# Performance work log

Measured on AMD Instinct MI355X. Metric: run time of the kernel, lower is better.

The kernel has to match this reference:

```python
import jax, jax.numpy as jnp
import numpy as np
from functools import partial

IM_H, IM_W = 1024, 1024
PRE_NMS = 1000
POST_NMS = 1000
FPN_POST_NMS = 1000
NMS_THRESH = 0.7
MIN_SIZE = 0.0
XFORM_CLIP = float(np.log(1000.0 / 16.0))  # BoxCoder bbox_xform_clip
K_MIN, K_MAX, K0, S0 = 2, 5, 4, 224.0      # ROI->FPN level mapper
NEG_INF = -1.0e30
N_IMG = 8


def _make_anchors(H, W, stride, n_img):
    """Grid anchors in H,W,A order (matches permute(0,2,3,1) flattening)."""
    ratios = np.array([0.5, 1.0, 2.0])
    size = stride * 8.0
    ws = size * np.sqrt(1.0 / ratios)
    hs = size * np.sqrt(ratios)
    sx = (np.arange(W) + 0.5) * stride
    sy = (np.arange(H) + 0.5) * stride
    cx, cy = np.meshgrid(sx, sy)  # [H,W]
    x1 = cx[..., None] - ws / 2.0
    y1 = cy[..., None] - hs / 2.0
    x2 = cx[..., None] + ws / 2.0
    y2 = cy[..., None] + hs / 2.0
    anc = np.stack([x1, y1, x2, y2], -1).reshape(-1, 4).astype(np.float32)
    return jnp.asarray(np.broadcast_to(anc, (n_img,) + anc.shape).copy())


def setup_inputs() -> dict:
    key = jax.random.key(0)
    ks = jax.random.split(key, 6)
    inp = {
        "obj_p2": jax.random.normal(ks[0], (N_IMG, 3, 256, 256), jnp.float32),
        "obj_p3": jax.random.normal(ks[1], (N_IMG, 3, 128, 128), jnp.float32),
        "obj_p4": jax.random.normal(ks[2], (N_IMG, 3, 64, 64), jnp.float32),
        "breg_p2": jax.random.normal(ks[3], (N_IMG, 12, 256, 256), jnp.float32) * 0.25,
        "breg_p3": jax.random.normal(ks[4], (N_IMG, 12, 128, 128), jnp.float32) * 0.25,
        "breg_p4": jax.random.normal(ks[5], (N_IMG, 12, 64, 64), jnp.float32) * 0.25,
        "anchors_p2": _make_anchors(256, 256, 4, N_IMG),
        "anchors_p3": _make_anchors(128, 128, 8, N_IMG),
        "anchors_p4": _make_anchors(64, 64, 16, N_IMG),
    }
    return inp


def _decode(deltas, anchors):
    # BoxCoder(weights=(1,1,1,1)) decode with the detectron +1 convention
    w = anchors[..., 2] - anchors[..., 0] + 1.0
    h = anchors[..., 3] - anchors[..., 1] + 1.0
    cx = anchors[..., 0] + 0.5 * w
    cy = anchors[..., 1] + 0.5 * h
    dx, dy = deltas[..., 0], deltas[..., 1]
    dw = jnp.minimum(deltas[..., 2], XFORM_CLIP)
    dh = jnp.minimum(deltas[..., 3], XFORM_CLIP)
    pcx = dx * w + cx
    pcy = dy * h + cy
    pw = jnp.exp(dw) * w
    ph = jnp.exp(dh) * h
    return jnp.stack(
        [pcx - 0.5 * pw, pcy - 0.5 * ph, pcx + 0.5 * pw - 1.0, pcy + 0.5 * ph - 1.0], -1
    )


def _nms_keep(boxes, valid, thresh):
    # boxes [K,4] already sorted by score desc; greedy hard NMS -> keep mask
    x1, y1, x2, y2 = boxes[:, 0], boxes[:, 1], boxes[:, 2], boxes[:, 3]
    areas = (x2 - x1 + 1.0) * (y2 - y1 + 1.0)
    xx1 = jnp.maximum(x1[:, None], x1[None, :])
    yy1 = jnp.maximum(y1[:, None], y1[None, :])
    xx2 = jnp.minimum(x2[:, None], x2[None, :])
    yy2 = jnp.minimum(y2[:, None], y2[None, :])
    inter = jnp.clip(xx2 - xx1 + 1.0, 0.0) * jnp.clip(yy2 - yy1 + 1.0, 0.0)
    iou = inter / (areas[:, None] + areas[None, :] - inter)
    K = boxes.shape[0]
    js = jnp.arange(K)

    def body(i, keep):
        sup = keep[i] & (iou[i] > thresh) & (js > i)
        return keep & ~sup

    return jax.lax.fori_loop(0, K, body, valid)


def _per_level(obj, breg, anchors):
    N, A, H, W = obj.shape
    scores = jax.nn.sigmoid(obj.transpose(0, 2, 3, 1).reshape(N, -1))  # [N, HWA]
    deltas = breg.reshape(N, A, 4, H, W).transpose(0, 3, 4, 1, 2).reshape(N, -1, 4)
    k = min(PRE_NMS, scores.shape[1])
    s, idx = jax.lax.top_k(scores, k)  # sorted desc
    d = jnp.take_along_axis(deltas, idx[..., None], axis=1)
    a = jnp.take_along_axis(anchors, idx[..., None], axis=1)
    p = _decode(d, a)
    # clip to image (width-1 / height-1)
    p = jnp.stack(
        [
            jnp.clip(p[..., 0], 0.0, IM_W - 1.0),
            jnp.clip(p[..., 1], 0.0, IM_H - 1.0),
            jnp.clip(p[..., 2], 0.0, IM_W - 1.0),
            jnp.clip(p[..., 3], 0.0, IM_H - 1.0),
        ],
        -1,
    )
    ws = p[..., 2] - p[..., 0] + 1.0
    hs = p[..., 3] - p[..., 1] + 1.0
    xc = p[..., 0] + ws / 2.0
    yc = p[..., 1] + hs / 2.0
    valid = (ws >= MIN_SIZE) & (hs >= MIN_SIZE) & (xc < IM_W) & (yc < IM_H)
    keep = jax.vmap(partial(_nms_keep, thresh=NMS_THRESH))(p, valid)
    ms = jnp.where(keep, s, NEG_INF)
    s2, i2 = jax.lax.top_k(ms, min(POST_NMS, k))
    b2 = jnp.take_along_axis(p, i2[..., None], axis=1)
    return b2, s2


def reference(obj_p2, obj_p3, obj_p4, breg_p2, breg_p3, breg_p4,
              anchors_p2, anchors_p3, anchors_p4):
    levels_in = [
        (obj_p2, breg_p2, anchors_p2),
        (obj_p3, breg_p3, anchors_p3),
        (obj_p4, breg_p4, anchors_p4),
    ]
    bs, ss = zip(*[_per_level(o, b, a) for o, b, a in levels_in])
    boxes = jnp.concatenate(bs, axis=1)   # [N, L*POST_NMS, 4]
    scores = jnp.concatenate(ss, axis=1)  # [N, L*POST_NMS]
    pk = min(FPN_POST_NMS, scores.shape[1])
    fs, fi = jax.lax.top_k(scores, pk)    # per-image inference-mode topk
    fb = jnp.take_along_axis(boxes, fi[..., None], axis=1)
    # ROI -> FPN level mapping
    area = (fb[..., 2] - fb[..., 0] + 1.0) * (fb[..., 3] - fb[..., 1] + 1.0)
    lvl = jnp.floor(K0 + jnp.log2(jnp.sqrt(area) / S0 + 1e-6))
    lvl = jnp.clip(lvl, K_MIN, K_MAX).astype(jnp.int32)
    return fb, fs, lvl
```

## Files before the change

kernel.cpp:

```cpp
#include <hip/hip_runtime.h>

#define NTASK 24
#define KSEL 1000
#define NIMG 8
#define NEG_INF_D (-1e30)
#define CAND_CAP 2048


static __device__ __forceinline__ unsigned fkey(float x) {
    unsigned u = __float_as_uint(x);
    return u ^ ((u >> 31) ? 0xFFFFFFFFu : 0x80000000u);
}

static __device__ __forceinline__ unsigned long long dkey(double d) {
    unsigned long long u = (unsigned long long)__double_as_longlong(d);
    if (u >> 63) u = ~u; else u |= 0x8000000000000000ull;
    return u;
}

static __device__ __forceinline__ int level_hw(int lvl) {
    return lvl == 0 ? 65536 : (lvl == 1 ? 16384 : 4096);
}


__global__ __launch_bounds__(256) void k_zero(uint4* __restrict__ p, int n16) {
    const int t = blockIdx.x * 256 + threadIdx.x;
    if (t < n16) p[t] = make_uint4(0u, 0u, 0u, 0u);
}


__global__ __launch_bounds__(256) void k_hist(const float* __restrict__ o2,
                                              const float* __restrict__ o3,
                                              const float* __restrict__ o4,
                                              unsigned* __restrict__ hist) {
    const int task = blockIdx.x, img = task / 3, lvl = task % 3;
    const float* obj = lvl == 0 ? o2 : (lvl == 1 ? o3 : o4);
    const int HW = level_hw(lvl);
    const int total = 3 * HW;
    const float* base = obj + (size_t)img * total;
    const int tid = threadIdx.x;

    __shared__ unsigned h[4096];
    for (int t = tid; t < 4096; t += 256) h[t] = 0u;
    __syncthreads();

    const int per = total / 32;
    const int beg = blockIdx.y * per;
    for (int t = beg + tid; t < beg + per; t += 256) {
        unsigned key = fkey(base[t]);
        atomicAdd(&h[key >> 20], 1u);
    }
    __syncthreads();

    unsigned* H = hist + task * 4096;
    for (int t = tid; t < 4096; t += 256)
        if (h[t]) atomicAdd(&H[t], h[t]);
}


__global__ __launch_bounds__(256) void k_thresh(const unsigned* __restrict__ hist,
                                                int* __restrict__ thrBin) {
    const int task = blockIdx.x, tid = threadIdx.x;
    __shared__ unsigned h[4096];
    __shared__ unsigned part[256];
    const unsigned* H = hist + task * 4096;
    for (int t = tid; t < 4096; t += 256) h[t] = H[t];
    __syncthreads();
    unsigned s = 0;
    for (int q = 0; q < 16; ++q) s += h[tid * 16 + q];
    part[tid] = s;
    __syncthreads();
    if (tid == 0) {
        unsigned cum = 0;
        int c = 255;
        for (; c >= 0; --c) {
            if (cum + part[c] >= (unsigned)KSEL) break;
            cum += part[c];
        }
        if (c < 0) c = 0;
        int bin = 0;
        for (int b = c * 16 + 15; b >= c * 16; --b) {
            if (cum + h[b] >= (unsigned)KSEL) { bin = b; break; }
            cum += h[b];
        }
        thrBin[task] = bin;
    }
}


__global__ __launch_bounds__(256) void k_compact(const float* __restrict__ o2,
                                                 const float* __restrict__ o3,
                                                 const float* __restrict__ o4,
                                                 const int* __restrict__ thrBin,
                                                 unsigned* __restrict__ cnt,
                                                 unsigned long long* __restrict__ cand) {
    const int task = blockIdx.x, img = task / 3, lvl = task % 3;
    const float* obj = lvl == 0 ? o2 : (lvl == 1 ? o3 : o4);
    const int HW = level_hw(lvl);
    const int total = 3 * HW;
    const float* base = obj + (size_t)img * total;
    const unsigned B = (unsigned)thrBin[task];

    __shared__ unsigned long long buf[CAND_CAP];
    __shared__ unsigned scnt, sbase;
    if (threadIdx.x == 0) scnt = 0u;
    __syncthreads();

    const int per = total / 32;
    const int per4 = per >> 2;
    const int beg4 = blockIdx.y * per4;
    const float4* base4 = (const float4*)base;
    for (int t = beg4 + threadIdx.x; t < beg4 + per4; t += 256) {
        float4 v = base4[t];
        const int e0 = t * 4;
#pragma unroll
        for (int q = 0; q < 4; ++q) {
            float x = q == 0 ? v.x : (q == 1 ? v.y : (q == 2 ? v.z : v.w));
            unsigned key = fkey(x);
            if ((key >> 20) >= B) {
                unsigned s = atomicAdd(&scnt, 1u);
                if (s < CAND_CAP) {
                    int el = e0 + q;
                    int a = el / HW, pos = el - a * HW;
                    int i = pos * 3 + a;
                    buf[s] = ((unsigned long long)key << 32) | (unsigned)(~(unsigned)i);
                }
            }
        }
    }
    __syncthreads();
    unsigned n = scnt; if (n > CAND_CAP) n = CAND_CAP;
    if (threadIdx.x == 0) sbase = atomicAdd(&cnt[task], n);
    __syncthreads();
    const unsigned b0 = sbase;
    for (unsigned t = threadIdx.x; t < n; t += 256) {
        unsigned slot = b0 + t;
        if (slot < CAND_CAP) cand[task * CAND_CAP + slot] = buf[t];
    }
}


__global__ __launch_bounds__(1024) void k_sel(const unsigned* __restrict__ cnt,
                                              const unsigned long long* __restrict__ cand,
                                              int* __restrict__ idx_out) {
    const int task = blockIdx.x, tid = threadIdx.x;
    __shared__ unsigned long long comp[CAND_CAP];
    int n = (int)cnt[task]; if (n > CAND_CAP) n = CAND_CAP;
    for (int t = tid; t < CAND_CAP; t += 1024)
        comp[t] = (t < n) ? cand[task * CAND_CAP + t] : 0ull;
    __syncthreads();

    for (unsigned k = 2; k <= CAND_CAP; k <<= 1) {
        for (unsigned j = k >> 1; j > 0; j >>= 1) {
            for (unsigned i = tid; i < CAND_CAP; i += 1024) {
                unsigned ixj = i ^ j;
                if (ixj > i) {
                    unsigned long long A = comp[i], Bv = comp[ixj];
                    bool desc = ((i & k) == 0);
                    if ((A < Bv) == desc) { comp[i] = Bv; comp[ixj] = A; }
                }
            }
            __syncthreads();
        }
    }

    for (int t = tid; t < KSEL; t += 1024)
        idx_out[task * KSEL + t] = (int)(~(unsigned)(comp[t] & 0xFFFFFFFFull));
}


__global__ __launch_bounds__(256) void k_decode(const float* __restrict__ o2, const float* __restrict__ o3, const float* __restrict__ o4,
                                                const float* __restrict__ g2, const float* __restrict__ g3, const float* __restrict__ g4,
                                                const float* __restrict__ a2, const float* __restrict__ a3, const float* __restrict__ a4,
                                                const int* __restrict__ idx,
                                                double* __restrict__ boxes, double* __restrict__ score, int* __restrict__ valid) {
    const int task = blockIdx.x, img = task / 3, lvl = task % 3;
    const float* obj = lvl == 0 ? o2 : (lvl == 1 ? o3 : o4);
    const float* brg = lvl == 0 ? g2 : (lvl == 1 ? g3 : g4);
    const float* anc = lvl == 0 ? a2 : (lvl == 1 ? a3 : a4);
    const int HW = level_hw(lvl);
    const int N = HW * 3;
    const double XC = 4.135166556742356;

    const int r = blockIdx.y * 250 + threadIdx.x;
    if (threadIdx.x < 250 && r < KSEL) {
        int i = idx[task * KSEL + r];
        int a = i % 3, pos = i / 3;
        double x = (double)obj[(size_t)img * 3 * HW + (size_t)a * HW + pos];
        double s = 1.0 / (1.0 + exp(-x));

        const float* bb = brg + (size_t)img * 12 * HW + (size_t)(a * 4) * HW + pos;
        double dx = (double)bb[0];
        double dy = (double)bb[(size_t)HW];
        double dw = (double)bb[(size_t)2 * HW];
        double dh = (double)bb[(size_t)3 * HW];

        const float* an = anc + ((size_t)img * N + (size_t)i) * 4;
        double ax1 = an[0], ay1 = an[1], ax2 = an[2], ay2 = an[3];

        double w = ax2 - ax1 + 1.0, h = ay2 - ay1 + 1.0;
        double cx = ax1 + 0.5 * w, cy = ay1 + 0.5 * h;
        if (dw > XC) dw = XC;
        if (dh > XC) dh = XC;
        double pcx = dx * w + cx, pcy = dy * h + cy;
        double pw = exp(dw) * w, ph = exp(dh) * h;
        double x1 = pcx - 0.5 * pw, y1 = pcy - 0.5 * ph;
        double x2 = pcx + 0.5 * pw - 1.0, y2 = pcy + 0.5 * ph - 1.0;
        x1 = fmin(fmax(x1, 0.0), 1023.0);
        y1 = fmin(fmax(y1, 0.0), 1023.0);
        x2 = fmin(fmax(x2, 0.0), 1023.0);
        y2 = fmin(fmax(y2, 0.0), 1023.0);
        double ws_ = x2 - x1 + 1.0, hs_ = y2 - y1 + 1.0;
        double xc = x1 + ws_ / 2.0, yc = y1 + hs_ / 2.0;
        int v = (ws_ >= 0.0) && (hs_ >= 0.0) && (xc < 1024.0) && (yc < 1024.0);

        double* bo = boxes + (size_t)(task * KSEL + r) * 4;
        bo[0] = x1; bo[1] = y1; bo[2] = x2; bo[3] = y2;
        score[task * KSEL + r] = s;
        valid[task * KSEL + r] = v;
    }
}


__global__ __launch_bounds__(512) void k_mask(const double* __restrict__ boxes,
                                              unsigned long long* __restrict__ maskT) {
    const int task = blockIdx.x;
    const int wid = threadIdx.x >> 6, lane = threadIdx.x & 63;
    const int t = blockIdx.y * 8 + wid;
    if (t >= 136) return;
    int I = 0, rem = t;
    while (rem >= 16 - I) { rem -= 16 - I; ++I; }
    const int J = I + rem;

    const double* B = boxes + (size_t)task * KSEL * 4;
    const int j = J * 64 + lane;
    const int jc = j < KSEL ? j : KSEL - 1;
    double jx1 = B[jc * 4 + 0], jy1 = B[jc * 4 + 1];
    double jx2 = B[jc * 4 + 2], jy2 = B[jc * 4 + 3];
    double aj = (jx2 - jx1 + 1.0) * (jy2 - jy1 + 1.0);

    unsigned long long* MT = maskT + (size_t)task * 16000 + (size_t)J * KSEL;
    int iend = I * 64 + 64; if (iend > KSEL) iend = KSEL;
    for (int i = I * 64; i < iend; ++i) {
        double ix1 = B[i * 4 + 0], iy1 = B[i * 4 + 1];
        double ix2 = B[i * 4 + 2], iy2 = B[i * 4 + 3];
        double ai = (ix2 - ix1 + 1.0) * (iy2 - iy1 + 1.0);
        double xx1 = fmax(ix1, jx1), yy1 = fmax(iy1, jy1);
        double xx2 = fmin(ix2, jx2), yy2 = fmin(iy2, jy2);
        double iw = xx2 - xx1 + 1.0; iw = iw > 0.0 ? iw : 0.0;
        double ih = yy2 - yy1 + 1.0; ih = ih > 0.0 ? ih : 0.0;
        double inter = iw * ih;
        double iou = inter / (ai + aj - inter);
        bool sup = (j > i) && (j < KSEL) && (iou > 0.7);
        unsigned long long m = __ballot(sup);
        if (lane == 0) MT[i] = m;
    }
}


__global__ __launch_bounds__(1024) void k_nms(const unsigned long long* __restrict__ maskT,
                                              const int* __restrict__ valid,
                                              const double* __restrict__ score,
                                              int* __restrict__ order, double* __restrict__ s2) {
    const int task = blockIdx.x;
    const int tid = threadIdx.x;
    const int wid = tid >> 6, lane = tid & 63;

    __shared__ unsigned long long Msh[16000];
    __shared__ unsigned long long kws[16];
    __shared__ int prefK[16], prefN[16], totKsh;

    {
        const ulonglong2* MG = (const ulonglong2*)(maskT + (size_t)task * 16000);
        ulonglong2* ML = (ulonglong2*)Msh;
        for (int t = tid; t < 8000; t += 1024) ML[t] = MG[t];
    }
    if (tid < 16) kws[tid] = 0ull;
    __syncthreads();
    if (tid < KSEL && valid[task * KSEL + tid])
        atomicOr(&kws[tid >> 6], 1ull << (tid & 63));
    __syncthreads();

    for (int p = 0; p < 16; ++p) {
        if (p > 0 && wid >= p) {
            unsigned long long kp = kws[p - 1];
            unsigned long long m = ((kp >> lane) & 1ull) ? Msh[wid * KSEL + (p - 1) * 64 + lane] : 0ull;
            if (m) atomicAnd(&kws[wid], ~m);
        }
        if (wid == p) {
            __threadfence_block();
            const int row = p * 64 + lane;
            unsigned long long m = (row < KSEL) ? Msh[p * KSEL + row] : 0ull;
            unsigned long long k = kws[p];
            unsigned long long processed = 0ull;
            while (true) {
                unsigned long long sup = __ballot((m & k) != 0ull);
                unsigned long long rem = k & sup & ~processed;
                if (!rem) break;
                int b = __ffsll((long long)rem) - 1;
                unsigned lo = (unsigned)__builtin_amdgcn_readlane((int)(unsigned)(m & 0xFFFFFFFFull), b);
                unsigned hi = (unsigned)__builtin_amdgcn_readlane((int)(unsigned)(m >> 32), b);
                unsigned long long vict = ((unsigned long long)hi << 32) | lo;
                k &= ~vict;
                processed = (1ull << b) | ((1ull << b) - 1ull);
            }
            if (lane == 0) kws[p] = k;
        }
        __syncthreads();
    }

    if (tid == 0) {
        int pk = 0, pn = 0;
        for (int l = 0; l < 16; ++l) {
            prefK[l] = pk; prefN[l] = pn;
            int limit = KSEL - 64 * l; if (limit > 64) limit = 64;
            int kb = (int)__popcll(kws[l]);
            pk += kb; pn += limit - kb;
        }
        totKsh = pk;
    }
    __syncthreads();

    if (tid < 16) {
        unsigned long long kw = kws[tid];
        int limit = KSEL - 64 * tid; if (limit > 64) limit = 64;
        int ck = prefK[tid], cn = totKsh + prefN[tid];
        for (int b = 0; b < limit; ++b) {
            int j = tid * 64 + b;
            if ((kw >> b) & 1ull) {
                order[task * KSEL + ck] = j;
                s2[task * KSEL + ck] = score[task * KSEL + j];
                ++ck;
            } else {
                order[task * KSEL + cn] = j;
                s2[task * KSEL + cn] = NEG_INF_D;
                ++cn;
            }
        }
    }
}


__global__ __launch_bounds__(1024) void k_final(const double* __restrict__ boxes,
                                                const double* __restrict__ s2,
                                                const int* __restrict__ order,
                                                float* __restrict__ out) {
    const int img = blockIdx.x;
    const int tid = threadIdx.x;
    __shared__ unsigned long long Mkey[KSEL];
    __shared__ int Mid[KSEL];

    const double* L0 = s2 + (size_t)(img * 3 + 0) * KSEL;
    const double* L1 = s2 + (size_t)(img * 3 + 1) * KSEL;
    const double* L2 = s2 + (size_t)(img * 3 + 2) * KSEL;

    if (tid < KSEL) {
        const int r = tid;
        int lo = 0, hi = r;
        while (lo < hi) {
            int a = (lo + hi) >> 1;
            if (dkey(L0[a]) >= dkey(L1[r - 1 - a])) lo = a + 1; else hi = a;
        }
        int a = lo, b = r - a;
        unsigned long long ka = dkey(L0[a]), kb = dkey(L1[b]);
        if (ka >= kb) { Mkey[r] = ka; Mid[r] = a; }
        else          { Mkey[r] = kb; Mid[r] = 1000 + b; }
    }
    __syncthreads();

    if (tid < KSEL) {
        const int r = tid;
        int lo = 0, hi = r;
        while (lo < hi) {
            int a = (lo + hi) >> 1;
            if (Mkey[a] >= dkey(L2[r - 1 - a])) lo = a + 1; else hi = a;
        }
        int a = lo, b = r - a;
        int e;
        if (a < KSEL && Mkey[a] >= dkey(L2[b])) e = Mid[a];
        else e = 2000 + b;

        int l = e / 1000, rr = e - l * 1000;
        int task = img * 3 + l;
        int pos = order[task * KSEL + rr];
        const double* bo = boxes + (size_t)(task * KSEL + pos) * 4;
        double b0 = bo[0], b1 = bo[1], b2 = bo[2], b3 = bo[3];
        double s = s2[task * KSEL + rr];

        float* fb = out + ((size_t)img * KSEL + r) * 4;
        fb[0] = (float)b0; fb[1] = (float)b1; fb[2] = (float)b2; fb[3] = (float)b3;
        out[8 * KSEL * 4 + img * KSEL + r] = (float)s;

        double area = (b2 - b0 + 1.0) * (b3 - b1 + 1.0);
        double lv = floor(4.0 + log2(sqrt(area) / 224.0 + 1e-6));
        if (!(lv >= 2.0)) lv = 2.0;
        if (lv > 5.0) lv = 5.0;
        out[8 * KSEL * 5 + img * KSEL + r] = (float)lv;
    }
}


extern "C" void kernel_launch(void* const* d_in, const int* in_sizes, int n_in,
                              void* d_out, int out_size, void* d_ws, size_t ws_size,
                              hipStream_t stream) {
    const float* o2 = (const float*)d_in[0];
    const float* o3 = (const float*)d_in[1];
    const float* o4 = (const float*)d_in[2];
    const float* g2 = (const float*)d_in[3];
    const float* g3 = (const float*)d_in[4];
    const float* g4 = (const float*)d_in[5];
    const float* a2 = (const float*)d_in[6];
    const float* a3 = (const float*)d_in[7];
    const float* a4 = (const float*)d_in[8];

    char* ws = (char*)d_ws;
    int*                idx   = (int*)(ws + 0);
    int*                valid = (int*)(ws + 96000);
    double*             score = (double*)(ws + 192000);
    double*             boxes = (double*)(ws + 384000);
    int*                order = (int*)(ws + 1152000);
    double*             s2    = (double*)(ws + 1248000);
    char*               scr   = ws + 1440000;

    unsigned*           hist   = (unsigned*)(scr + 0);
    unsigned*           cnt    = (unsigned*)(scr + 393216);
    int*                thrBin = (int*)(scr + 393312);
    unsigned long long* cand   = (unsigned long long*)(scr + 393472);
    unsigned long long* maskT  = (unsigned long long*)scr;

    k_zero<<<97, 256, 0, stream>>>((uint4*)scr, 24582);

    k_hist<<<dim3(NTASK, 32), 256, 0, stream>>>(o2, o3, o4, hist);
    k_thresh<<<NTASK, 256, 0, stream>>>(hist, thrBin);
    k_compact<<<dim3(NTASK, 32), 256, 0, stream>>>(o2, o3, o4, thrBin, cnt, cand);
    k_sel<<<NTASK, 1024, 0, stream>>>(cnt, cand, idx);

    k_decode<<<dim3(NTASK, 4), 256, 0, stream>>>(o2, o3, o4, g2, g3, g4, a2, a3, a4,
                                                 idx, boxes, score, valid);
    k_mask<<<dim3(NTASK, 17), 512, 0, stream>>>(boxes, maskT);
    k_nms<<<NTASK, 1024, 0, stream>>>(maskT, valid, score, order, s2);
    k_final<<<NIMG, 1024, 0, stream>>>(boxes, s2, order, (float*)d_out);
}
```

Measured before the change: 122.7 us.

## Fuse threshold into histogram and selection into decode, use per-segment candidate buffers

The threshold computation moves into the histogram kernel: the last block per task, detected with a done counter and threadfence, finds the threshold bin. The histogram now reads float4 loads. Compaction writes each block's candidates to its own fixed segment, replacing the shared global atomic slot. Sort and decode are merged into one kernel that rebuilds each score from its sort key instead of re-reading the objectness tensor. This removes two kernel launches and some global round-trips, but any block with more than 192 candidates now silently drops the extras.

```diff
diff --git a/kernel.cpp b/kernel.cpp
--- a/kernel.cpp
+++ b/kernel.cpp
@@ -4,12 +4,18 @@
 #define KSEL 1000
 #define NIMG 8
 #define NEG_INF_D (-1e30)
-#define CAND_CAP 2048
+#define SEG 192
+#define SORTN 2048
 
 
 static __device__ __forceinline__ unsigned fkey(float x) {
     unsigned u = __float_as_uint(x);
     return u ^ ((u >> 31) ? 0xFFFFFFFFu : 0x80000000u);
+}
+
+static __device__ __forceinline__ float fkey_inv(unsigned key) {
+    unsigned u = (key >> 31) ? (key ^ 0x80000000u) : ~key;
+    return __uint_as_float(u);
 }
 
 static __device__ __forceinline__ unsigned long long dkey(double d) {
@@ -32,7 +38,9 @@
 __global__ __launch_bounds__(256) void k_hist(const float* __restrict__ o2,
                                               const float* __restrict__ o3,
                                               const float* __restrict__ o4,
-                                              unsigned* __restrict__ hist) {
+                                              unsigned* __restrict__ hist,
+                                              unsigned* __restrict__ done,
+                                              int* __restrict__ thrBin) {
     const int task = blockIdx.x, img = task / 3, lvl = task % 3;
     const float* obj = lvl == 0 ? o2 : (lvl == 1 ? o3 : o4);
     const int HW = level_hw(lvl);
@@ -41,30 +49,34 @@
     const int tid = threadIdx.x;
 
     __shared__ unsigned h[4096];
+    __shared__ unsigned part[256];
+    __shared__ int lastFlag;
+
     for (int t = tid; t < 4096; t += 256) h[t] = 0u;
     __syncthreads();
 
-    const int per = total / 32;
-    const int beg = blockIdx.y * per;
-    for (int t = beg + tid; t < beg + per; t += 256) {
-        unsigned key = fkey(base[t]);
-        atomicAdd(&h[key >> 20], 1u);
+    const int per4 = (total / 32) >> 2;
+    const int beg4 = blockIdx.y * per4;
+    const float4* base4 = (const float4*)base;
+    for (int t = beg4 + tid; t < beg4 + per4; t += 256) {
+        float4 v = base4[t];
+        atomicAdd(&h[fkey(v.x) >> 20], 1u);
+        atomicAdd(&h[fkey(v.y) >> 20], 1u);
+        atomicAdd(&h[fkey(v.z) >> 20], 1u);
+        atomicAdd(&h[fkey(v.w) >> 20], 1u);
     }
     __syncthreads();
 
     unsigned* H = hist + task * 4096;
     for (int t = tid; t < 4096; t += 256)
         if (h[t]) atomicAdd(&H[t], h[t]);
-}
-
-
-__global__ __launch_bounds__(256) void k_thresh(const unsigned* __restrict__ hist,
-                                                int* __restrict__ thrBin) {
-    const int task = blockIdx.x, tid = threadIdx.x;
-    __shared__ unsigned h[4096];
-    __shared__ unsigned part[256];
-    const unsigned* H = hist + task * 4096;
-    for (int t = tid; t < 4096; t += 256) h[t] = H[t];
+
+    __threadfence();
+    if (tid == 0) lastFlag = (atomicAdd(&done[task], 1u) == 31u);
+    __syncthreads();
+    if (!lastFlag) return;
+
+    for (int t = tid; t < 4096; t += 256) h[t] = atomicAdd(&H[t], 0u);
     __syncthreads();
     unsigned s = 0;
     for (int q = 0; q < 16; ++q) s += h[tid * 16 + q];
@@ -92,7 +104,7 @@
                                                  const float* __restrict__ o3,
                                                  const float* __restrict__ o4,
                                                  const int* __restrict__ thrBin,
-                                                 unsigned* __restrict__ cnt,
+                                                 int* __restrict__ cntB,
                                                  unsigned long long* __restrict__ cand) {
     const int task = blockIdx.x, img = task / 3, lvl = task % 3;
     const float* obj = lvl == 0 ? o2 : (lvl == 1 ? o3 : o4);
@@ -101,13 +113,12 @@
     const float* base = obj + (size_t)img * total;
     const unsigned B = (unsigned)thrBin[task];
 
-    __shared__ unsigned long long buf[CAND_CAP];
-    __shared__ unsigned scnt, sbase;
+    __shared__ unsigned long long buf[256];
+    __shared__ unsigned scnt;
     if (threadIdx.x == 0) scnt = 0u;
     __syncthreads();
 
-    const int per = total / 32;
-    const int per4 = per >> 2;
+    const int per4 = (total / 32) >> 2;
     const int beg4 = blockIdx.y * per4;
     const float4* base4 = (const float4*)base;
     for (int t = beg4 + threadIdx.x; t < beg4 + per4; t += 256) {
@@ -119,7 +130,7 @@
             unsigned key = fkey(x);
             if ((key >> 20) >= B) {
                 unsigned s = atomicAdd(&scnt, 1u);
-                if (s < CAND_CAP) {
+                if (s < 256u) {
                     int el = e0 + q;
                     int a = el / HW, pos = el - a * HW;
                     int i = pos * 3 + a;
@@ -129,30 +140,44 @@
         }
     }
     __syncthreads();
-    unsigned n = scnt; if (n > CAND_CAP) n = CAND_CAP;
-    if (threadIdx.x == 0) sbase = atomicAdd(&cnt[task], n);
-    __syncthreads();
-    const unsigned b0 = sbase;
-    for (unsigned t = threadIdx.x; t < n; t += 256) {
-        unsigned slot = b0 + t;
-        if (slot < CAND_CAP) cand[task * CAND_CAP + slot] = buf[t];
-    }
-}
-
-
-__global__ __launch_bounds__(1024) void k_sel(const unsigned* __restrict__ cnt,
-                                              const unsigned long long* __restrict__ cand,
-                                              int* __restrict__ idx_out) {
-    const int task = blockIdx.x, tid = threadIdx.x;
-    __shared__ unsigned long long comp[CAND_CAP];
-    int n = (int)cnt[task]; if (n > CAND_CAP) n = CAND_CAP;
-    for (int t = tid; t < CAND_CAP; t += 1024)
-        comp[t] = (t < n) ? cand[task * CAND_CAP + t] : 0ull;
-    __syncthreads();
-
-    for (unsigned k = 2; k <= CAND_CAP; k <<= 1) {
+    int n = (int)scnt; if (n > SEG) n = SEG;
+    const int seg = task * 32 + blockIdx.y;
+    if (threadIdx.x == 0) cntB[seg] = n;
+    unsigned long long* C = cand + (size_t)seg * SEG;
+    for (int t = threadIdx.x; t < n; t += 256) C[t] = buf[t];
+}
+
+
+__global__ __launch_bounds__(1024) void k_seldec(
+    const int* __restrict__ cntB, const unsigned long long* __restrict__ cand,
+    const float* __restrict__ g2, const float* __restrict__ g3, const float* __restrict__ g4,
+    const float* __restrict__ a2, const float* __restrict__ a3, const float* __restrict__ a4,
+    double* __restrict__ boxes, double* __restrict__ score, int* __restrict__ valid) {
+
+    const int task = blockIdx.x, img = task / 3, lvl = task % 3;
+    const int tid = threadIdx.x;
+    __shared__ unsigned long long comp[SORTN];
+    __shared__ int pref[33];
+
+    if (tid == 0) {
+        int p = 0;
+        for (int s = 0; s < 32; ++s) { pref[s] = p; p += cntB[task * 32 + s]; }
+        pref[32] = p;
+    }
+    for (int t = tid; t < SORTN; t += 1024) comp[t] = 0ull;
+    __syncthreads();
+
+    for (int s = 0; s < 32; ++s) {
+        const int b = pref[s], n = pref[s + 1] - b;
+        const unsigned long long* C = cand + (size_t)(task * 32 + s) * SEG;
+        for (int k = tid; k < n; k += 1024)
+            if (b + k < SORTN) comp[b + k] = C[k];
+    }
+    __syncthreads();
+
+    for (unsigned k = 2; k <= SORTN; k <<= 1) {
         for (unsigned j = k >> 1; j > 0; j >>= 1) {
-            for (unsigned i = tid; i < CAND_CAP; i += 1024) {
+            for (unsigned i = tid; i < SORTN; i += 1024) {
                 unsigned ixj = i ^ j;
                 if (ixj > i) {
                     unsigned long long A = comp[i], Bv = comp[ixj];
@@ -164,29 +189,19 @@
         }
     }
 
-    for (int t = tid; t < KSEL; t += 1024)
-        idx_out[task * KSEL + t] = (int)(~(unsigned)(comp[t] & 0xFFFFFFFFull));
-}
-
-
-__global__ __launch_bounds__(256) void k_decode(const float* __restrict__ o2, const float* __restrict__ o3, const float* __restrict__ o4,
-                                                const float* __restrict__ g2, const float* __restrict__ g3, const float* __restrict__ g4,
-                                                const float* __restrict__ a2, const float* __restrict__ a3, const float* __restrict__ a4,
-                                                const int* __restrict__ idx,
-                                                double* __restrict__ boxes, double* __restrict__ score, int* __restrict__ valid) {
-    const int task = blockIdx.x, img = task / 3, lvl = task % 3;
-    const float* obj = lvl == 0 ? o2 : (lvl == 1 ? o3 : o4);
-    const float* brg = lvl == 0 ? g2 : (lvl == 1 ? g3 : g4);
-    const float* anc = lvl == 0 ? a2 : (lvl == 1 ? a3 : a4);
-    const int HW = level_hw(lvl);
-    const int N = HW * 3;
-    const double XC = 4.135166556742356;
-
-    const int r = blockIdx.y * 250 + threadIdx.x;
-    if (threadIdx.x < 250 && r < KSEL) {
-        int i = idx[task * KSEL + r];
+    if (tid < KSEL) {
+        const float* brg = lvl == 0 ? g2 : (lvl == 1 ? g3 : g4);
+        const float* anc = lvl == 0 ? a2 : (lvl == 1 ? a3 : a4);
+        const int HW = level_hw(lvl);
+        const int N = HW * 3;
+        const double XC = 4.135166556742356;
+
+        unsigned long long e = comp[tid];
+        unsigned key = (unsigned)(e >> 32);
+        int i = (int)(~(unsigned)(e & 0xFFFFFFFFull));
         int a = i % 3, pos = i / 3;
-        double x = (double)obj[(size_t)img * 3 * HW + (size_t)a * HW + pos];
+
+        double x = (double)fkey_inv(key);
         double s = 1.0 / (1.0 + exp(-x));
 
         const float* bb = brg + (size_t)img * 12 * HW + (size_t)(a * 4) * HW + pos;
@@ -214,10 +229,10 @@
         double xc = x1 + ws_ / 2.0, yc = y1 + hs_ / 2.0;
         int v = (ws_ >= 0.0) && (hs_ >= 0.0) && (xc < 1024.0) && (yc < 1024.0);
 
-        double* bo = boxes + (size_t)(task * KSEL + r) * 4;
+        double* bo = boxes + (size_t)(task * KSEL + tid) * 4;
         bo[0] = x1; bo[1] = y1; bo[2] = x2; bo[3] = y2;
-        score[task * KSEL + r] = s;
-        valid[task * KSEL + r] = v;
+        score[task * KSEL + tid] = s;
+        valid[task * KSEL + tid] = v;
     }
 }
 
@@ -414,7 +429,6 @@
     const float* a4 = (const float*)d_in[8];
 
     char* ws = (char*)d_ws;
-    int*                idx   = (int*)(ws + 0);
     int*                valid = (int*)(ws + 96000);
     double*             score = (double*)(ws + 192000);
     double*             boxes = (double*)(ws + 384000);
@@ -423,20 +437,18 @@
     char*               scr   = ws + 1440000;
 
     unsigned*           hist   = (unsigned*)(scr + 0);
-    unsigned*           cnt    = (unsigned*)(scr + 393216);
+    unsigned*           done   = (unsigned*)(scr + 393216);
     int*                thrBin = (int*)(scr + 393312);
-    unsigned long long* cand   = (unsigned long long*)(scr + 393472);
+    int*                cntB   = (int*)(scr + 393408);
+    unsigned long long* cand   = (unsigned long long*)(scr + 396480);
     unsigned long long* maskT  = (unsigned long long*)scr;
 
     k_zero<<<97, 256, 0, stream>>>((uint4*)scr, 24582);
 
-    k_hist<<<dim3(NTASK, 32), 256, 0, stream>>>(o2, o3, o4, hist);
-    k_thresh<<<NTASK, 256, 0, stream>>>(hist, thrBin);
-    k_compact<<<dim3(NTASK, 32), 256, 0, stream>>>(o2, o3, o4, thrBin, cnt, cand);
-    k_sel<<<NTASK, 1024, 0, stream>>>(cnt, cand, idx);
-
-    k_decode<<<dim3(NTASK, 4), 256, 0, stream>>>(o2, o3, o4, g2, g3, g4, a2, a3, a4,
-                                                 idx, boxes, score, valid);
+    k_hist<<<dim3(NTASK, 32), 256, 0, stream>>>(o2, o3, o4, hist, done, thrBin);
+    k_compact<<<dim3(NTASK, 32), 256, 0, stream>>>(o2, o3, o4, thrBin, cntB, cand);
+    k_seldec<<<NTASK, 1024, 0, stream>>>(cntB, cand, g2, g3, g4, a2, a3, a4,
+                                         boxes, score, valid);
     k_mask<<<dim3(NTASK, 17), 512, 0, stream>>>(boxes, maskT);
     k_nms<<<NTASK, 1024, 0, stream>>>(maskT, valid, score, order, s2);
     k_final<<<NIMG, 1024, 0, stream>>>(boxes, s2, order, (float*)d_out);
```

New measurement: 171.2 us. 1.4x slower.
